# Kernel optimization log

Measured on AMD Instinct MI355X. Metric: run time of the kernel, lower is better.

The kernel has to match this reference:

```python
import jax, jax.numpy as jnp
import numpy as np

WS = 8       # window size per axis
SHIFT = 4    # cyclic shift per axis
NH = 12      # attention heads
EPS = 1e-6


def _ln(x):
    # LayerNorm, elementwise_affine=False, eps=1e-6
    m = jnp.mean(x, axis=-1, keepdims=True)
    v = jnp.mean((x - m) ** 2, axis=-1, keepdims=True)
    return (x - m) * jax.lax.rsqrt(v + EPS)


def setup_inputs() -> dict:
    key = jax.random.key(0)
    ks = jax.random.split(key, 8)
    N, T, C = 8, 4096, 768
    HID = 3072
    s = 0.02
    return {
        "x_seq": jax.random.normal(ks[0], (N, T, C), jnp.float32),
        "c": jax.random.normal(ks[1], (N, C), jnp.float32),
        "qkv_w": jax.random.normal(ks[2], (3 * C, C), jnp.float32) * s,
        "qkv_b": jnp.zeros((3 * C,), jnp.float32),
        "proj_w": jax.random.normal(ks[3], (C, C), jnp.float32) * s,
        "proj_b": jnp.zeros((C,), jnp.float32),
        "fc1_w": jax.random.normal(ks[4], (HID, C), jnp.float32) * s,
        "fc1_b": jnp.zeros((HID,), jnp.float32),
        "fc2_w": jax.random.normal(ks[5], (C, HID), jnp.float32) * s,
        "fc2_b": jnp.zeros((C,), jnp.float32),
        "ada_w": jax.random.normal(ks[6], (6 * C, C), jnp.float32) * s,
        "ada_b": jnp.zeros((6 * C,), jnp.float32),
        "H": 64,
        "W": 64,
    }


def reference(x_seq, c, qkv_w, qkv_b, proj_w, proj_b,
              fc1_w, fc1_b, fc2_w, fc2_b, ada_w, ada_b, H, W):
    N, T, C = x_seq.shape
    hd = C // NH

    # adaLN-Zero conditioning: SiLU -> Linear(dim, 6*dim) -> chunk(6)
    ada = jax.nn.silu(c) @ ada_w.T + ada_b                    # (N, 6C)
    sh_msa, sc_msa, g_msa, sh_mlp, sc_mlp, g_mlp = jnp.split(ada, 6, axis=1)

    # to grid, cyclic shift (grid divisible by window -> pads are zero)
    x = x_seq.reshape(N, H, W, C)
    x = jnp.roll(x, (-SHIFT, -SHIFT), axis=(1, 2))

    nh, nw = H // WS, W // WS
    nWin = nh * nw
    Tw = WS * WS
    # window partition: (N, nh, WS, nw, WS, C) -> (N*nWin, Tw, C)
    xw = x.reshape(N, nh, WS, nw, WS, C).transpose(0, 1, 3, 2, 4, 5)
    xw = xw.reshape(N * nWin, Tw, C)

    # repeat adaLN params per-window (repeat_interleave along batch)
    shm = jnp.repeat(sh_msa, nWin, axis=0)
    scm = jnp.repeat(sc_msa, nWin, axis=0)
    gm = jnp.repeat(g_msa, nWin, axis=0)

    h = _ln(xw)
    h = h * (1.0 + scm[:, None, :]) + shm[:, None, :]

    # window attention (qkv_bias=True)
    qkv = h @ qkv_w.T + qkv_b                                  # (B_, Tw, 3C)
    qkv = qkv.reshape(-1, Tw, 3, NH, hd).transpose(2, 0, 3, 1, 4)
    q, k, v = qkv[0], qkv[1], qkv[2]                           # (B_, NH, Tw, hd)
    att = jnp.einsum('bhqd,bhkd->bhqk', q, k) / jnp.sqrt(jnp.float32(hd))
    att = jax.nn.softmax(att, axis=-1)
    out = jnp.einsum('bhqk,bhkd->bhqd', att, v)
    out = out.transpose(0, 2, 1, 3).reshape(-1, Tw, C)
    out = out @ proj_w.T + proj_b

    xw = xw + gm[:, None, :] * out

    # window unpartition + inverse shift
    x = xw.reshape(N, nh, nw, WS, WS, C).transpose(0, 1, 3, 2, 4, 5)
    x = x.reshape(N, H, W, C)
    x = jnp.roll(x, (SHIFT, SHIFT), axis=(1, 2)).reshape(N, T, C)

    # MLP branch with adaLN
    h = _ln(x)
    h = h * (1.0 + sc_mlp[:, None, :]) + sh_mlp[:, None, :]
    h = jax.nn.gelu(h @ fc1_w.T + fc1_b, approximate=True) @ fc2_w.T + fc2_b
    return x + g_mlp[:, None, :] * h
```

## Files before the change

### kernel.cpp

```cpp
#include <hip/hip_runtime.h>
#include <stdint.h>

typedef __attribute__((ext_vector_type(8))) __bf16 bf16x8;
typedef __attribute__((ext_vector_type(4))) float f32x4;
typedef __attribute__((ext_vector_type(4))) unsigned short u16x4;
typedef unsigned short u16;

__device__ __forceinline__ float bf2f(u16 u) {
  union { unsigned int i; float f; } x; x.i = ((unsigned int)u) << 16; return x.f;
}
__device__ __forceinline__ u16 f2bf(float f) {
  union { float f; unsigned int i; } x; x.f = f;
  unsigned int r = (x.i + 0x7fffu + ((x.i >> 16) & 1u)) >> 16;
  return (u16)r;
}

__device__ __forceinline__ void async16(void* lds, const void* g) {
  __builtin_amdgcn_global_load_lds((__attribute__((address_space(1))) void*)g,
                                   (__attribute__((address_space(3))) void*)lds,
                                   16, 0, 0);
}

__global__ __launch_bounds__(256)
void sniff_k(const u16* __restrict__ x, int* __restrict__ flag) {
  __shared__ int cnt;
  if (threadIdx.x == 0) cnt = 0;
  __syncthreads();
  int good = 0;
  for (int i = threadIdx.x; i < 512; i += 256) {
    int e = (x[i] >> 7) & 0xFF;
    good += (e >= 110 && e <= 130) ? 1 : 0;
  }
  atomicAdd(&cnt, good);
  __syncthreads();
  if (threadIdx.x == 0) *flag = (cnt >= 448) ? 0 : 1;
}

__global__ __launch_bounds__(256)
void conv_k(const void* __restrict__ src, u16* __restrict__ dst, int n,
            const int* __restrict__ flag) {
  const int md = *flag;
  int i = blockIdx.x * 256 + threadIdx.x;
  const int stride = gridDim.x * 256;
  if (md) {
    const float* s = (const float*)src;
    for (; i < n; i += stride) dst[i] = f2bf(s[i]);
  } else {
    const u16* s = (const u16*)src;
    for (; i < n; i += stride) dst[i] = s[i];
  }
}

__global__ __launch_bounds__(256)
void ada_k(const u16* __restrict__ c, const u16* __restrict__ aw,
           const u16* __restrict__ ab, float* __restrict__ ada) {
  int gw = blockIdx.x * 4 + (threadIdx.x >> 6);
  int lane = threadIdx.x & 63;
  int n = gw / 4608, j = gw - n * 4608;
  const u16* cr = c + n * 768;
  const u16* wr = aw + (long)j * 768;
  float s = 0.f;
#pragma unroll
  for (int i = 0; i < 12; i++) {
    int k = lane + i * 64;
    float cv = bf2f(cr[k]);
    cv = cv / (1.f + __expf(-cv));
    s += cv * bf2f(wr[k]);
  }
  for (int off = 32; off > 0; off >>= 1) s += __shfl_xor(s, off);
  if (lane == 0) ada[(long)n * 4608 + j] = s + bf2f(ab[j]);
}

template<int MODE>
__global__ __launch_bounds__(256)
void ln_mod(const void* __restrict__ src, const float* __restrict__ ada,
            u16* __restrict__ out, const int* __restrict__ flag) {
  const int md = (MODE == 0) ? *flag : 0;
  int m = blockIdx.x * 4 + (threadIdx.x >> 6);
  int lane = threadIdx.x & 63;
  int n; long soff;
  if (MODE == 0) {
    int b = m >> 6, t = m & 63;
    n = b >> 6;
    int wi = b & 63;
    int hh = ((wi >> 3) << 3) + (t >> 3);
    int ww = ((wi & 7) << 3) + (t & 7);
    int oh = (hh + 4) & 63, ow = (ww + 4) & 63;
    soff = ((long)n * 4096 + oh * 64 + ow) * 768;
  } else {
    n = m >> 12;
    soff = (long)m * 768;
  }
  const u16* su = (const u16*)src;
  const float* sf = (const float*)src;
  float vals[12];
  float s1 = 0.f, s2 = 0.f;
#pragma unroll
  for (int i = 0; i < 12; i++) {
    long idx = soff + lane + i * 64;
    float v = (MODE == 0 && md) ? sf[idx] : bf2f(su[idx]);
    vals[i] = v; s1 += v; s2 += v * v;
  }
  for (int off = 32; off > 0; off >>= 1) { s1 += __shfl_xor(s1, off); s2 += __shfl_xor(s2, off); }
  float mean = s1 * (1.f / 768.f);
  float var = s2 * (1.f / 768.f) - mean * mean;
  float rstd = rsqrtf(var + 1e-6f);
  const float* ap = ada + (long)n * 4608 + (MODE == 0 ? 0 : 2304);
#pragma unroll
  for (int i = 0; i < 12; i++) {
    int ch = lane + i * 64;
    float sh = ap[ch], sc = ap[768 + ch];
    out[(long)m * 768 + ch] = f2bf((vals[i] - mean) * rstd * (1.f + sc) + sh);
  }
}

__device__ __forceinline__ bf16x8 ldsRead(const char* region, int rowb, int quad) {
  int D = rowb * 64 + quad * 16;
  D ^= ((D >> 7) & 7) << 4;
  return *(const bf16x8*)(region + D);
}

__device__ __forceinline__ void stage_half(const u16* __restrict__ G, long row0,
                                           int K, int kbase, char* region,
                                           int wave, int tid) {
#pragma unroll
  for (int rr = 0; rr < 2; rr++) {
    const int D = rr * 8192 + tid * 16;
    const int S = D ^ (((D >> 7) & 7) << 4);
    async16(region + rr * 8192 + wave * 1024,
            G + (row0 + (S >> 6)) * (long)K + (kbase + ((S & 63) >> 1)));
  }
}

__device__ __forceinline__ void ck8() { asm volatile("s_waitcnt vmcnt(8)"); }
__device__ __forceinline__ void ck4() { asm volatile("s_waitcnt vmcnt(4)"); }
__device__ __forceinline__ void ck0() { asm volatile("s_waitcnt vmcnt(0)"); }

#define MFMA_(a, b, c) __builtin_amdgcn_mfma_f32_16x16x32_bf16(a, b, c, 0, 0, 0)
#define NOP_ ((void)0)

#define PHASE(MH, AR, BR, STAGE_EXPR, CKPT_EXPR) do {                          \
    if ((MH) == 0) {                                                           \
      bf[0] = ldsRead((BR), wcb + 0  + l16, quad);                             \
      bf[1] = ldsRead((BR), wcb + 16 + l16, quad);                             \
      bf[2] = ldsRead((BR), wcb + 32 + l16, quad);                             \
      bf[3] = ldsRead((BR), wcb + 48 + l16, quad);                             \
    }                                                                          \
    bf16x8 af0 = ldsRead((AR), wrb + (MH)*64 + 0  + l16, quad);                \
    bf16x8 af1 = ldsRead((AR), wrb + (MH)*64 + 16 + l16, quad);                \
    bf16x8 af2 = ldsRead((AR), wrb + (MH)*64 + 32 + l16, quad);                \
    bf16x8 af3 = ldsRead((AR), wrb + (MH)*64 + 48 + l16, quad);                \
    STAGE_EXPR;                                                                \
    CKPT_EXPR;                                                                 \
    asm volatile("s_barrier" ::: "memory");                                    \
    asm volatile("s_waitcnt lgkmcnt(0)");                                      \
    __builtin_amdgcn_sched_barrier(0);                                         \
    __builtin_amdgcn_s_setprio(1);                                             \
    acc[(MH)*4+0][0] = MFMA_(af0, bf[0], acc[(MH)*4+0][0]);                    \
    acc[(MH)*4+0][1] = MFMA_(af0, bf[1], acc[(MH)*4+0][1]);                    \
    acc[(MH)*4+0][2] = MFMA_(af0, bf[2], acc[(MH)*4+0][2]);                    \
    acc[(MH)*4+0][3] = MFMA_(af0, bf[3], acc[(MH)*4+0][3]);                    \
    acc[(MH)*4+1][0] = MFMA_(af1, bf[0], acc[(MH)*4+1][0]);                    \
    acc[(MH)*4+1][1] = MFMA_(af1, bf[1], acc[(MH)*4+1][1]);                    \
    acc[(MH)*4+1][2] = MFMA_(af1, bf[2], acc[(MH)*4+1][2]);                    \
    acc[(MH)*4+1][3] = MFMA_(af1, bf[3], acc[(MH)*4+1][3]);                    \
    acc[(MH)*4+2][0] = MFMA_(af2, bf[0], acc[(MH)*4+2][0]);                    \
    acc[(MH)*4+2][1] = MFMA_(af2, bf[1], acc[(MH)*4+2][1]);                    \
    acc[(MH)*4+2][2] = MFMA_(af2, bf[2], acc[(MH)*4+2][2]);                    \
    acc[(MH)*4+2][3] = MFMA_(af2, bf[3], acc[(MH)*4+2][3]);                    \
    acc[(MH)*4+3][0] = MFMA_(af3, bf[0], acc[(MH)*4+3][0]);                    \
    acc[(MH)*4+3][1] = MFMA_(af3, bf[1], acc[(MH)*4+3][1]);                    \
    acc[(MH)*4+3][2] = MFMA_(af3, bf[2], acc[(MH)*4+3][2]);                    \
    acc[(MH)*4+3][3] = MFMA_(af3, bf[3], acc[(MH)*4+3][3]);                    \
    __builtin_amdgcn_s_setprio(0);                                             \
    __builtin_amdgcn_sched_barrier(0);                                         \
    asm volatile("s_barrier" ::: "memory");                                    \
  } while (0)

template<int EPI>
__global__ __launch_bounds__(512, 1)
void gemm_bt(const u16* __restrict__ A, const u16* __restrict__ W,
             const u16* __restrict__ bias, void* __restrict__ outb,
             int K, int O,
             const float* __restrict__ ada, const void* __restrict__ resid,
             long m0, const int* __restrict__ flag) {
  const int md = (EPI >= 2) ? *flag : 0;
  __shared__ __align__(16) u16 As[4 * 8192];
  __shared__ __align__(16) u16 Bs[4 * 8192];
  const int tid = threadIdx.x;
  const int wave = tid >> 6, lane = tid & 63;
  const int quad = lane >> 4, l16 = lane & 15;
  const int wr = wave >> 2, wc = wave & 3;
  const int wrb = wr * 128, wcb = wc * 64;

  const int gx = gridDim.x;
  const int nwg = gx * (int)gridDim.y;
  int id = (int)blockIdx.y * gx + (int)blockIdx.x;
  {
    const int q8 = nwg >> 3, r8 = nwg & 7;
    const int xcd = id & 7, loc = id >> 3;
    id = (xcd < r8 ? xcd * (q8 + 1) : r8 * (q8 + 1) + (xcd - r8) * q8) + loc;
  }
  const int ty = id / gx, tx = id - ty * gx;
  const long tile_m = (long)ty * 256;
  const int tile_o = tx * 256;

  char* AsB = (char*)As;
  char* BsB = (char*)Bs;
  const int NKT = K >> 6;

  stage_half(A, tile_m, K, 0,  AsB + 0 * 16384, wave, tid);
  stage_half(W, tile_o, K, 0,  BsB + 0 * 16384, wave, tid);
  stage_half(A, tile_m, K, 32, AsB + 1 * 16384, wave, tid);
  stage_half(W, tile_o, K, 32, BsB + 1 * 16384, wave, tid);
  stage_half(A, tile_m, K, 64, AsB + 2 * 16384, wave, tid);
  stage_half(W, tile_o, K, 64, BsB + 2 * 16384, wave, tid);
  ck8();
  asm volatile("s_barrier" ::: "memory");

  f32x4 acc[8][4] = {};
  bf16x8 bf[4];

  int t = 0;
  for (; t <= NKT - 3; ++t) {
    const int buf = t & 1;
    const char* Ar0 = AsB + ((buf << 1) | 0) * 16384;
    const char* Br0 = BsB + ((buf << 1) | 0) * 16384;
    const char* Ar1 = AsB + ((buf << 1) | 1) * 16384;
    const char* Br1 = BsB + ((buf << 1) | 1) * 16384;
    char* pa1 = AsB + (((buf ^ 1) << 1) | 1) * 16384;
    char* pb1 = BsB + (((buf ^ 1) << 1) | 1) * 16384;
    char* pa0 = AsB + ((buf << 1) | 0) * 16384;
    char* pb0 = BsB + ((buf << 1) | 0) * 16384;
    PHASE(0, Ar0, Br0, (stage_half(A, tile_m, K, (t + 1) * 64 + 32, pa1, wave, tid)), NOP_);
    PHASE(1, Ar0, Br0, (stage_half(W, tile_o, K, (t + 1) * 64 + 32, pb1, wave, tid)), ck8());
    PHASE(0, Ar1, Br1, (stage_half(A, tile_m, K, (t + 2) * 64,      pa0, wave, tid)), NOP_);
    PHASE(1, Ar1, Br1, (stage_half(W, tile_o, K, (t + 2) * 64,      pb0, wave, tid)), ck8());
  }
  {
    const int buf = t & 1;
    const char* Ar0 = AsB + ((buf << 1) | 0) * 16384;
    const char* Br0 = BsB + ((buf << 1) | 0) * 16384;
    const char* Ar1 = AsB + ((buf << 1) | 1) * 16384;
    const char* Br1 = BsB + ((buf << 1) | 1) * 16384;
    char* pa1 = AsB + (((buf ^ 1) << 1) | 1) * 16384;
    char* pb1 = BsB + (((buf ^ 1) << 1) | 1) * 16384;
    PHASE(0, Ar0, Br0, (stage_half(A, tile_m, K, (t + 1) * 64 + 32, pa1, wave, tid)), NOP_);
    PHASE(1, Ar0, Br0, (stage_half(W, tile_o, K, (t + 1) * 64 + 32, pb1, wave, tid)), ck8());
    PHASE(0, Ar1, Br1, NOP_, NOP_);
    PHASE(1, Ar1, Br1, NOP_, ck4());
    t++;
  }
  {
    const int buf = t & 1;
    const char* Ar0 = AsB + ((buf << 1) | 0) * 16384;
    const char* Br0 = BsB + ((buf << 1) | 0) * 16384;
    const char* Ar1 = AsB + ((buf << 1) | 1) * 16384;
    const char* Br1 = BsB + ((buf << 1) | 1) * 16384;
    PHASE(0, Ar0, Br0, NOP_, NOP_);
    PHASE(1, Ar0, Br0, NOP_, ck0());
    PHASE(0, Ar1, Br1, NOP_, NOP_);
    PHASE(1, Ar1, Br1, NOP_, NOP_);
  }

  float* sAf = (float*)As;
  float* sBf = (float*)Bs;
  const int colq = lane * 4;
  const int gcol = tile_o + colq;
  const u16x4 bq = *(const u16x4*)&bias[gcol];
#pragma unroll
  for (int p = 0; p < 2; p++) {
    if (p) asm volatile("s_barrier" ::: "memory");
    if (wr == p) {
#pragma unroll
      for (int mi = 0; mi < 8; mi++) {
        float* rg = (mi < 4) ? sAf : sBf;
#pragma unroll
        for (int ni = 0; ni < 4; ni++) {
#pragma unroll
          for (int r = 0; r < 4; r++) {
            const int row = mi * 16 + quad * 4 + r;
            const int colS = (wcb + ni * 16 + l16) ^ (quad << 4);
            rg[((row & 63) << 8) + colS] = acc[mi][ni][r];
          }
        }
      }
    }
    asm volatile("s_waitcnt lgkmcnt(0)" ::: "memory");
    asm volatile("s_barrier" ::: "memory");
#pragma unroll
    for (int it = 0; it < 16; it++) {
      const int row = it * 8 + wave;
      const float* rg = (row < 64) ? sAf : sBf;
      const int colS = colq ^ (((row >> 2) & 3) << 4);
      f32x4 v4 = *(const f32x4*)&rg[((row & 63) << 8) + colS];
      const long mrow = tile_m + (long)p * 128 + row;
      float vv[4];
#pragma unroll
      for (int j = 0; j < 4; j++) vv[j] = v4[j] + bf2f(bq[j]);
      if (EPI == 0) {
        u16x4 o4;
#pragma unroll
        for (int j = 0; j < 4; j++) o4[j] = f2bf(vv[j]);
        __builtin_nontemporal_store(o4, (u16x4*)((u16*)outb + mrow * O + gcol));
      } else if (EPI == 1) {
        u16x4 o4;
#pragma unroll
        for (int j = 0; j < 4; j++) {
          float v = vv[j];
          float tt = v + 0.044715f * v * v * v;
          o4[j] = f2bf(0.5f * v * (1.f + tanhf(0.79788456080286536f * tt)));
        }
        __builtin_nontemporal_store(o4, (u16x4*)((u16*)outb + mrow * O + gcol));
      } else if (EPI == 2) {
        const int m = (int)mrow;
        const int b = m >> 6, tk = m & 63;
        const int n = b >> 6, wi = b & 63;
        const int hh = ((wi >> 3) << 3) + (tk >> 3);
        const int ww = ((wi & 7) << 3) + (tk & 7);
        const int oh = (hh + 4) & 63, ow = (ww + 4) & 63;
        const long dst = ((long)n * 4096 + oh * 64 + ow) * 768 + gcol;
        const f32x4 gm = *(const f32x4*)&ada[(long)n * 4608 + 1536 + gcol];
        u16x4 o4;
        if (md) {
          f32x4 rv = __builtin_nontemporal_load((const f32x4*)((const float*)resid + dst));
#pragma unroll
          for (int j = 0; j < 4; j++) o4[j] = f2bf(rv[j] + gm[j] * vv[j]);
        } else {
          u16x4 rv = __builtin_nontemporal_load((const u16x4*)((const u16*)resid + dst));
#pragma unroll
          for (int j = 0; j < 4; j++) o4[j] = f2bf(bf2f(rv[j]) + gm[j] * vv[j]);
        }
        __builtin_nontemporal_store(o4, (u16x4*)((u16*)outb + dst));
      } else {
        const long mg = m0 + mrow;
        const int n = (int)(mg >> 12);
        const long dst = mg * 768 + gcol;
        const f32x4 gm = *(const f32x4*)&ada[(long)n * 4608 + 3840 + gcol];
        u16x4 rv = __builtin_nontemporal_load((const u16x4*)((const u16*)resid + dst));
        if (md) {
          f32x4 ov;
#pragma unroll
          for (int j = 0; j < 4; j++) ov[j] = bf2f(rv[j]) + gm[j] * vv[j];
          __builtin_nontemporal_store(ov, (f32x4*)((float*)outb + dst));
        } else {
          u16x4 o4;
#pragma unroll
          for (int j = 0; j < 4; j++) o4[j] = f2bf(bf2f(rv[j]) + gm[j] * vv[j]);
          __builtin_nontemporal_store(o4, (u16x4*)((u16*)outb + dst));
        }
      }
    }
  }
}

__global__ __launch_bounds__(256)
void attn_k(const u16* __restrict__ qkv, u16* __restrict__ out) {
  const int h = blockIdx.x, b = blockIdx.y;
  __shared__ u16 qs[64 * 66];
  __shared__ u16 kt[64 * 66];
  __shared__ u16 vs[64 * 66];
  __shared__ float ps[64 * 65];
  const int tid = threadIdx.x;
  const u16* base = qkv + (long)b * 64 * 2304 + h * 64;
#pragma unroll
  for (int i = 0; i < 16; i++) {
    int t = (tid >> 6) + i * 4;
    int d = tid & 63;
    qs[t * 66 + d] = base[(long)t * 2304 + d];
    kt[d * 66 + t] = base[(long)t * 2304 + 768 + d];
    vs[t * 66 + d] = base[(long)t * 2304 + 1536 + d];
  }
  __syncthreads();
  const int r = tid >> 2, g = tid & 3;
  float s[16];
#pragma unroll
  for (int j = 0; j < 16; j++) s[j] = 0.f;
  for (int kk = 0; kk < 64; kk++) {
    float qv = bf2f(qs[r * 66 + kk]);
    const u16* krow = &kt[kk * 66 + g * 16];
#pragma unroll
    for (int j = 0; j < 16; j++) s[j] += qv * bf2f(krow[j]);
  }
  float mx = -1e30f;
#pragma unroll
  for (int j = 0; j < 16; j++) { s[j] *= 0.125f; mx = fmaxf(mx, s[j]); }
  mx = fmaxf(mx, __shfl_xor(mx, 1));
  mx = fmaxf(mx, __shfl_xor(mx, 2));
  float sum = 0.f;
#pragma unroll
  for (int j = 0; j < 16; j++) { s[j] = __expf(s[j] - mx); sum += s[j]; }
  sum += __shfl_xor(sum, 1);
  sum += __shfl_xor(sum, 2);
  float inv = 1.f / sum;
#pragma unroll
  for (int j = 0; j < 16; j++) ps[r * 65 + g * 16 + j] = s[j] * inv;
  __syncthreads();
  float o[16];
#pragma unroll
  for (int j = 0; j < 16; j++) o[j] = 0.f;
  for (int j = 0; j < 64; j++) {
    float pv = ps[r * 65 + j];
    const u16* vrow = &vs[j * 66 + g * 16];
#pragma unroll
    for (int d = 0; d < 16; d++) o[d] += pv * bf2f(vrow[d]);
  }
  u16* orow = out + ((long)b * 64 + r) * 768 + h * 64 + g * 16;
#pragma unroll
  for (int d = 0; d < 16; d++) orow[d] = f2bf(o[d]);
}

extern "C" void kernel_launch(void* const* d_in, const int* in_sizes, int n_in,
                              void* d_out, int out_size, void* d_ws, size_t ws_size,
                              hipStream_t stream) {
  const void* x_seq  = d_in[0];
  const void* c      = d_in[1];
  const void* qkv_w  = d_in[2];
  const void* qkv_b  = d_in[3];
  const void* proj_w = d_in[4];
  const void* proj_b = d_in[5];
  const void* fc1_w  = d_in[6];
  const void* fc1_b  = d_in[7];
  const void* fc2_w  = d_in[8];
  const void* fc2_b  = d_in[9];
  const void* ada_w  = d_in[10];
  const void* ada_b  = d_in[11];

  const size_t NEEDED = 222743056;
  if (ws_size < NEEDED) return;

  char* ws = (char*)d_ws;
  float* ada = (float*)(ws);
  int* flag  = (int*)(ws + 147456);
  u16* bufA  = (u16*)(ws + 147472);
  u16* bufB  = (u16*)(ws + 50479120);
  u16* xres  = (u16*)(ws + 151142416);
  u16* wbuf  = (u16*)(ws + 201474064);

  u16* w_c     = wbuf;
  u16* w_qkvw  = wbuf + 6144;
  u16* w_qkvb  = wbuf + 1775616;
  u16* w_projw = wbuf + 1777920;
  u16* w_projb = wbuf + 2367744;
  u16* w_fc1w  = wbuf + 2368512;
  u16* w_fc1b  = wbuf + 4727808;
  u16* w_fc2w  = wbuf + 4730880;
  u16* w_fc2b  = wbuf + 7090176;
  u16* w_adaw  = wbuf + 7090944;
  u16* w_adab  = wbuf + 10629888;

  sniff_k<<<1, 256, 0, stream>>>((const u16*)x_seq, flag);
  auto cv = [&](const void* s, u16* d, int n) {
    int blocks = (n + 2047) / 2048; if (blocks < 1) blocks = 1;
    conv_k<<<blocks, 256, 0, stream>>>(s, d, n, flag);
  };
  cv(c, w_c, 6144);
  cv(qkv_w, w_qkvw, 1769472);   cv(qkv_b, w_qkvb, 2304);
  cv(proj_w, w_projw, 589824);  cv(proj_b, w_projb, 768);
  cv(fc1_w, w_fc1w, 2359296);   cv(fc1_b, w_fc1b, 3072);
  cv(fc2_w, w_fc2w, 2359296);   cv(fc2_b, w_fc2b, 768);
  cv(ada_w, w_adaw, 3538944);   cv(ada_b, w_adab, 4608);

  ada_k<<<9216, 256, 0, stream>>>(w_c, w_adaw, w_adab, ada);
  ln_mod<0><<<8192, 256, 0, stream>>>(x_seq, ada, bufA, flag);
  for (int k2 = 0; k2 < 2; k2++) {
    const u16* hc = bufA + (long)k2 * 16384 * 768;
    gemm_bt<0><<<dim3(9, 64), 512, 0, stream>>>(hc, w_qkvw, w_qkvb, bufB,
                                                768, 2304, nullptr, nullptr, 0, flag);
    attn_k<<<dim3(12, 256), 256, 0, stream>>>(bufB, bufA + (long)k2 * 16384 * 768);
  }
  gemm_bt<2><<<dim3(3, 128), 512, 0, stream>>>(bufA, w_projw, w_projb, xres,
                                               768, 768, ada, x_seq, 0, flag);
  ln_mod<1><<<8192, 256, 0, stream>>>(xres, ada, bufA, flag);
  for (int cidx = 0; cidx < 2; cidx++) {
    const u16* h2c = bufA + (long)cidx * 16384 * 768;
    gemm_bt<1><<<dim3(12, 64), 512, 0, stream>>>(h2c, w_fc1w, w_fc1b, bufB,
                                                 768, 3072, nullptr, nullptr, 0, flag);
    gemm_bt<3><<<dim3(3, 64), 512, 0, stream>>>(bufB, w_fc2w, w_fc2b, d_out,
                                                3072, 768, ada, xres,
                                                (long)cidx * 16384, flag);
  }
}
```

Baseline: 1.385 ms.

## Halve GEMM LDS footprint to allow two workgroups per CU

Replaces the 4-slot, two-phase-per-half pipelined main loop with a simple double-buffered loop over 32-wide K slices, halving LDS for A and B tiles. The launch bounds now request two 512-thread blocks per CU so a second workgroup can hide latency instead of intra-block prefetch depth. The epilogue is reorganised into four 64-row passes to fit the smaller LDS. Risks: register pressure with 2 blocks/CU (128 acc floats plus 12 fragments), shallower prefetch, and a full vmcnt(0) wait plus barrier every K step.

```diff
diff --git a/kernel.cpp b/kernel.cpp
--- a/kernel.cpp
+++ b/kernel.cpp
@@ -132,61 +132,20 @@
   }
 }
 
-__device__ __forceinline__ void ck8() { asm volatile("s_waitcnt vmcnt(8)"); }
-__device__ __forceinline__ void ck4() { asm volatile("s_waitcnt vmcnt(4)"); }
 __device__ __forceinline__ void ck0() { asm volatile("s_waitcnt vmcnt(0)"); }
 
 #define MFMA_(a, b, c) __builtin_amdgcn_mfma_f32_16x16x32_bf16(a, b, c, 0, 0, 0)
-#define NOP_ ((void)0)
-
-#define PHASE(MH, AR, BR, STAGE_EXPR, CKPT_EXPR) do {                          \
-    if ((MH) == 0) {                                                           \
-      bf[0] = ldsRead((BR), wcb + 0  + l16, quad);                             \
-      bf[1] = ldsRead((BR), wcb + 16 + l16, quad);                             \
-      bf[2] = ldsRead((BR), wcb + 32 + l16, quad);                             \
-      bf[3] = ldsRead((BR), wcb + 48 + l16, quad);                             \
-    }                                                                          \
-    bf16x8 af0 = ldsRead((AR), wrb + (MH)*64 + 0  + l16, quad);                \
-    bf16x8 af1 = ldsRead((AR), wrb + (MH)*64 + 16 + l16, quad);                \
-    bf16x8 af2 = ldsRead((AR), wrb + (MH)*64 + 32 + l16, quad);                \
-    bf16x8 af3 = ldsRead((AR), wrb + (MH)*64 + 48 + l16, quad);                \
-    STAGE_EXPR;                                                                \
-    CKPT_EXPR;                                                                 \
-    asm volatile("s_barrier" ::: "memory");                                    \
-    asm volatile("s_waitcnt lgkmcnt(0)");                                      \
-    __builtin_amdgcn_sched_barrier(0);                                         \
-    __builtin_amdgcn_s_setprio(1);                                             \
-    acc[(MH)*4+0][0] = MFMA_(af0, bf[0], acc[(MH)*4+0][0]);                    \
-    acc[(MH)*4+0][1] = MFMA_(af0, bf[1], acc[(MH)*4+0][1]);                    \
-    acc[(MH)*4+0][2] = MFMA_(af0, bf[2], acc[(MH)*4+0][2]);                    \
-    acc[(MH)*4+0][3] = MFMA_(af0, bf[3], acc[(MH)*4+0][3]);                    \
-    acc[(MH)*4+1][0] = MFMA_(af1, bf[0], acc[(MH)*4+1][0]);                    \
-    acc[(MH)*4+1][1] = MFMA_(af1, bf[1], acc[(MH)*4+1][1]);                    \
-    acc[(MH)*4+1][2] = MFMA_(af1, bf[2], acc[(MH)*4+1][2]);                    \
-    acc[(MH)*4+1][3] = MFMA_(af1, bf[3], acc[(MH)*4+1][3]);                    \
-    acc[(MH)*4+2][0] = MFMA_(af2, bf[0], acc[(MH)*4+2][0]);                    \
-    acc[(MH)*4+2][1] = MFMA_(af2, bf[1], acc[(MH)*4+2][1]);                    \
-    acc[(MH)*4+2][2] = MFMA_(af2, bf[2], acc[(MH)*4+2][2]);                    \
-    acc[(MH)*4+2][3] = MFMA_(af2, bf[3], acc[(MH)*4+2][3]);                    \
-    acc[(MH)*4+3][0] = MFMA_(af3, bf[0], acc[(MH)*4+3][0]);                    \
-    acc[(MH)*4+3][1] = MFMA_(af3, bf[1], acc[(MH)*4+3][1]);                    \
-    acc[(MH)*4+3][2] = MFMA_(af3, bf[2], acc[(MH)*4+3][2]);                    \
-    acc[(MH)*4+3][3] = MFMA_(af3, bf[3], acc[(MH)*4+3][3]);                    \
-    __builtin_amdgcn_s_setprio(0);                                             \
-    __builtin_amdgcn_sched_barrier(0);                                         \
-    asm volatile("s_barrier" ::: "memory");                                    \
-  } while (0)
 
 template<int EPI>
-__global__ __launch_bounds__(512, 1)
+__global__ __launch_bounds__(512, 2)
 void gemm_bt(const u16* __restrict__ A, const u16* __restrict__ W,
              const u16* __restrict__ bias, void* __restrict__ outb,
              int K, int O,
              const float* __restrict__ ada, const void* __restrict__ resid,
              long m0, const int* __restrict__ flag) {
   const int md = (EPI >= 2) ? *flag : 0;
-  __shared__ __align__(16) u16 As[4 * 8192];
-  __shared__ __align__(16) u16 Bs[4 * 8192];
+  __shared__ __align__(16) u16 As[2 * 8192];
+  __shared__ __align__(16) u16 Bs[2 * 8192];
   const int tid = threadIdx.x;
   const int wave = tid >> 6, lane = tid & 63;
   const int quad = lane >> 4, l16 = lane & 15;
@@ -207,60 +166,74 @@
 
   char* AsB = (char*)As;
   char* BsB = (char*)Bs;
-  const int NKT = K >> 6;
-
-  stage_half(A, tile_m, K, 0,  AsB + 0 * 16384, wave, tid);
-  stage_half(W, tile_o, K, 0,  BsB + 0 * 16384, wave, tid);
-  stage_half(A, tile_m, K, 32, AsB + 1 * 16384, wave, tid);
-  stage_half(W, tile_o, K, 32, BsB + 1 * 16384, wave, tid);
-  stage_half(A, tile_m, K, 64, AsB + 2 * 16384, wave, tid);
-  stage_half(W, tile_o, K, 64, BsB + 2 * 16384, wave, tid);
-  ck8();
+  const int NKT = K >> 5;
+
+  stage_half(A, tile_m, K, 0, AsB, wave, tid);
+  stage_half(W, tile_o, K, 0, BsB, wave, tid);
+  ck0();
   asm volatile("s_barrier" ::: "memory");
 
   f32x4 acc[8][4] = {};
-  bf16x8 bf[4];
-
-  int t = 0;
-  for (; t <= NKT - 3; ++t) {
+
+  for (int t = 0; t < NKT; ++t) {
     const int buf = t & 1;
-    const char* Ar0 = AsB + ((buf << 1) | 0) * 16384;
-    const char* Br0 = BsB + ((buf << 1) | 0) * 16384;
-    const char* Ar1 = AsB + ((buf << 1) | 1) * 16384;
-    const char* Br1 = BsB + ((buf << 1) | 1) * 16384;
-    char* pa1 = AsB + (((buf ^ 1) << 1) | 1) * 16384;
-    char* pb1 = BsB + (((buf ^ 1) << 1) | 1) * 16384;
-    char* pa0 = AsB + ((buf << 1) | 0) * 16384;
-    char* pb0 = BsB + ((buf << 1) | 0) * 16384;
-    PHASE(0, Ar0, Br0, (stage_half(A, tile_m, K, (t + 1) * 64 + 32, pa1, wave, tid)), NOP_);
-    PHASE(1, Ar0, Br0, (stage_half(W, tile_o, K, (t + 1) * 64 + 32, pb1, wave, tid)), ck8());
-    PHASE(0, Ar1, Br1, (stage_half(A, tile_m, K, (t + 2) * 64,      pa0, wave, tid)), NOP_);
-    PHASE(1, Ar1, Br1, (stage_half(W, tile_o, K, (t + 2) * 64,      pb0, wave, tid)), ck8());
-  }
-  {
-    const int buf = t & 1;
-    const char* Ar0 = AsB + ((buf << 1) | 0) * 16384;
-    const char* Br0 = BsB + ((buf << 1) | 0) * 16384;
-    const char* Ar1 = AsB + ((buf << 1) | 1) * 16384;
-    const char* Br1 = BsB + ((buf << 1) | 1) * 16384;
-    char* pa1 = AsB + (((buf ^ 1) << 1) | 1) * 16384;
-    char* pb1 = BsB + (((buf ^ 1) << 1) | 1) * 16384;
-    PHASE(0, Ar0, Br0, (stage_half(A, tile_m, K, (t + 1) * 64 + 32, pa1, wave, tid)), NOP_);
-    PHASE(1, Ar0, Br0, (stage_half(W, tile_o, K, (t + 1) * 64 + 32, pb1, wave, tid)), ck8());
-    PHASE(0, Ar1, Br1, NOP_, NOP_);
-    PHASE(1, Ar1, Br1, NOP_, ck4());
-    t++;
-  }
-  {
-    const int buf = t & 1;
-    const char* Ar0 = AsB + ((buf << 1) | 0) * 16384;
-    const char* Br0 = BsB + ((buf << 1) | 0) * 16384;
-    const char* Ar1 = AsB + ((buf << 1) | 1) * 16384;
-    const char* Br1 = BsB + ((buf << 1) | 1) * 16384;
-    PHASE(0, Ar0, Br0, NOP_, NOP_);
-    PHASE(1, Ar0, Br0, NOP_, ck0());
-    PHASE(0, Ar1, Br1, NOP_, NOP_);
-    PHASE(1, Ar1, Br1, NOP_, NOP_);
+    const char* Ar = AsB + buf * 16384;
+    const char* Br = BsB + buf * 16384;
+    if (t + 1 < NKT) {
+      stage_half(A, tile_m, K, (t + 1) * 32, AsB + (buf ^ 1) * 16384, wave, tid);
+      stage_half(W, tile_o, K, (t + 1) * 32, BsB + (buf ^ 1) * 16384, wave, tid);
+    }
+    bf16x8 bf0 = ldsRead(Br, wcb + 0  + l16, quad);
+    bf16x8 bf1 = ldsRead(Br, wcb + 16 + l16, quad);
+    bf16x8 bf2 = ldsRead(Br, wcb + 32 + l16, quad);
+    bf16x8 bf3 = ldsRead(Br, wcb + 48 + l16, quad);
+    bf16x8 af0 = ldsRead(Ar, wrb + 0   + l16, quad);
+    bf16x8 af1 = ldsRead(Ar, wrb + 16  + l16, quad);
+    bf16x8 af2 = ldsRead(Ar, wrb + 32  + l16, quad);
+    bf16x8 af3 = ldsRead(Ar, wrb + 48  + l16, quad);
+    bf16x8 af4 = ldsRead(Ar, wrb + 64  + l16, quad);
+    bf16x8 af5 = ldsRead(Ar, wrb + 80  + l16, quad);
+    bf16x8 af6 = ldsRead(Ar, wrb + 96  + l16, quad);
+    bf16x8 af7 = ldsRead(Ar, wrb + 112 + l16, quad);
+    asm volatile("s_waitcnt lgkmcnt(0)");
+    __builtin_amdgcn_sched_barrier(0);
+    __builtin_amdgcn_s_setprio(1);
+    acc[0][0] = MFMA_(af0, bf0, acc[0][0]);
+    acc[0][1] = MFMA_(af0, bf1, acc[0][1]);
+    acc[0][2] = MFMA_(af0, bf2, acc[0][2]);
+    acc[0][3] = MFMA_(af0, bf3, acc[0][3]);
+    acc[1][0] = MFMA_(af1, bf0, acc[1][0]);
+    acc[1][1] = MFMA_(af1, bf1, acc[1][1]);
+    acc[1][2] = MFMA_(af1, bf2, acc[1][2]);
+    acc[1][3] = MFMA_(af1, bf3, acc[1][3]);
+    acc[2][0] = MFMA_(af2, bf0, acc[2][0]);
+    acc[2][1] = MFMA_(af2, bf1, acc[2][1]);
+    acc[2][2] = MFMA_(af2, bf2, acc[2][2]);
+    acc[2][3] = MFMA_(af2, bf3, acc[2][3]);
+    acc[3][0] = MFMA_(af3, bf0, acc[3][0]);
+    acc[3][1] = MFMA_(af3, bf1, acc[3][1]);
+    acc[3][2] = MFMA_(af3, bf2, acc[3][2]);
+    acc[3][3] = MFMA_(af3, bf3, acc[3][3]);
+    acc[4][0] = MFMA_(af4, bf0, acc[4][0]);
+    acc[4][1] = MFMA_(af4, bf1, acc[4][1]);
+    acc[4][2] = MFMA_(af4, bf2, acc[4][2]);
+    acc[4][3] = MFMA_(af4, bf3, acc[4][3]);
+    acc[5][0] = MFMA_(af5, bf0, acc[5][0]);
+    acc[5][1] = MFMA_(af5, bf1, acc[5][1]);
+    acc[5][2] = MFMA_(af5, bf2, acc[5][2]);
+    acc[5][3] = MFMA_(af5, bf3, acc[5][3]);
+    acc[6][0] = MFMA_(af6, bf0, acc[6][0]);
+    acc[6][1] = MFMA_(af6, bf1, acc[6][1]);
+    acc[6][2] = MFMA_(af6, bf2, acc[6][2]);
+    acc[6][3] = MFMA_(af6, bf3, acc[6][3]);
+    acc[7][0] = MFMA_(af7, bf0, acc[7][0]);
+    acc[7][1] = MFMA_(af7, bf1, acc[7][1]);
+    acc[7][2] = MFMA_(af7, bf2, acc[7][2]);
+    acc[7][3] = MFMA_(af7, bf3, acc[7][3]);
+    __builtin_amdgcn_s_setprio(0);
+    __builtin_amdgcn_sched_barrier(0);
+    ck0();
+    asm volatile("s_barrier" ::: "memory");
   }
 
   float* sAf = (float*)As;
@@ -269,19 +242,21 @@
   const int gcol = tile_o + colq;
   const u16x4 bq = *(const u16x4*)&bias[gcol];
 #pragma unroll
-  for (int p = 0; p < 2; p++) {
+  for (int p = 0; p < 4; p++) {
     if (p) asm volatile("s_barrier" ::: "memory");
-    if (wr == p) {
-#pragma unroll
-      for (int mi = 0; mi < 8; mi++) {
-        float* rg = (mi < 4) ? sAf : sBf;
+    if (wr == (p >> 1)) {
+      const int mi0 = (p & 1) * 4;
+#pragma unroll
+      for (int mm = 0; mm < 4; mm++) {
+        const int mi = mi0 + mm;
 #pragma unroll
         for (int ni = 0; ni < 4; ni++) {
 #pragma unroll
           for (int r = 0; r < 4; r++) {
-            const int row = mi * 16 + quad * 4 + r;
+            const int lr = mm * 16 + quad * 4 + r;
             const int colS = (wcb + ni * 16 + l16) ^ (quad << 4);
-            rg[((row & 63) << 8) + colS] = acc[mi][ni][r];
+            float* rg = (lr < 32) ? sAf : sBf;
+            rg[((lr & 31) << 8) + colS] = acc[mi][ni][r];
           }
         }
       }
@@ -289,12 +264,12 @@
     asm volatile("s_waitcnt lgkmcnt(0)" ::: "memory");
     asm volatile("s_barrier" ::: "memory");
 #pragma unroll
-    for (int it = 0; it < 16; it++) {
+    for (int it = 0; it < 8; it++) {
       const int row = it * 8 + wave;
-      const float* rg = (row < 64) ? sAf : sBf;
+      const float* rg = (row < 32) ? sAf : sBf;
       const int colS = colq ^ (((row >> 2) & 3) << 4);
-      f32x4 v4 = *(const f32x4*)&rg[((row & 63) << 8) + colS];
-      const long mrow = tile_m + (long)p * 128 + row;
+      f32x4 v4 = *(const f32x4*)&rg[((row & 31) << 8) + colS];
+      const long mrow = tile_m + (long)p * 64 + row;
       float vv[4];
 #pragma unroll
       for (int j = 0; j < 4; j++) vv[j] = v4[j] + bf2f(bq[j]);
```

Measured after the change: 1.450 ms. 1.05x slower.
